# Kernel optimization log

Measured on AMD Instinct MI355X. Metric: run time of the kernel, lower is better.

The kernel has to match this reference:

```python
import jax, jax.numpy as jnp
import numpy as np

N, E, G = 5000, 10000, 200
EPS = 1e-5


def _nnconv(x, edge_attr, src, dst, w1, b1, w2, b2, root, bias, din, dout):
    # edge MLP -> per-edge weight matrix [E, din, dout]
    h = jax.nn.relu(edge_attr @ w1 + b1)
    We = (h @ w2 + b2).reshape(-1, din, dout)
    # gather source node feats, per-edge bmm, scatter-mean to targets
    msg = jnp.einsum('ei,eio->eo', x[src], We)  # [E, dout]
    s = jax.ops.segment_sum(msg, dst, num_segments=N)
    cnt = jax.ops.segment_sum(jnp.ones((msg.shape[0],), msg.dtype), dst, num_segments=N)
    agg = s / jnp.maximum(cnt, 1.0)[:, None]
    return agg + x @ root + bias


def _bn(x, g, b, m, v):
    return (x - m) * (g / jnp.sqrt(v + EPS)) + b


def setup_inputs() -> dict:
    key = jax.random.key(0)
    ks = iter(jax.random.split(key, 64))
    d = {}
    d['x'] = jax.random.normal(next(ks), (N, 15), jnp.float32)
    d['edge_attr'] = jax.random.normal(next(ks), (E, 3), jnp.float32)
    d['edge_index'] = jax.random.randint(next(ks), (2, E), 0, N, jnp.int32)
    d['batch'] = jnp.sort(jax.random.randint(next(ks), (N,), 0, G, jnp.int32))
    d['atom_num'] = jnp.zeros((G,), jnp.int32)
    dims = [(15, 64), (64, 128), (128, 256)]
    for l, (din, dout) in enumerate(dims, start=1):
        d[f'nn{l}_w1'] = jax.random.normal(next(ks), (3, 32), jnp.float32) * 0.1
        d[f'nn{l}_b1'] = jnp.zeros((32,), jnp.float32)
        d[f'nn{l}_w2'] = jax.random.normal(next(ks), (32, din * dout), jnp.float32) * 0.05
        d[f'nn{l}_b2'] = jnp.zeros((din * dout,), jnp.float32)
        d[f'root{l}'] = jax.random.normal(next(ks), (din, dout), jnp.float32) * 0.1
        d[f'bias{l}'] = jnp.zeros((dout,), jnp.float32)
        d[f'bn{l}_g'] = jnp.ones((dout,), jnp.float32)
        d[f'bn{l}_b'] = jnp.zeros((dout,), jnp.float32)
        d[f'bn{l}_m'] = jnp.zeros((dout,), jnp.float32)
        d[f'bn{l}_v'] = jnp.ones((dout,), jnp.float32)
    d['mlp_w'] = jax.random.normal(next(ks), (256, 200), jnp.float32) * 0.05
    d['mlp_b'] = jnp.zeros((200,), jnp.float32)
    return d


def reference(x, edge_attr, edge_index, batch, atom_num,
              nn1_w1, nn1_b1, nn1_w2, nn1_b2, root1, bias1, bn1_g, bn1_b, bn1_m, bn1_v,
              nn2_w1, nn2_b1, nn2_w2, nn2_b2, root2, bias2, bn2_g, bn2_b, bn2_m, bn2_v,
              nn3_w1, nn3_b1, nn3_w2, nn3_b2, root3, bias3, bn3_g, bn3_b, bn3_m, bn3_v,
              mlp_w, mlp_b):
    src, dst = edge_index[0], edge_index[1]
    h = _nnconv(x, edge_attr, src, dst, nn1_w1, nn1_b1, nn1_w2, nn1_b2, root1, bias1, 15, 64)
    h = jax.nn.relu(_bn(h, bn1_g, bn1_b, bn1_m, bn1_v))
    h = _nnconv(h, edge_attr, src, dst, nn2_w1, nn2_b1, nn2_w2, nn2_b2, root2, bias2, 64, 128)
    h = jax.nn.relu(_bn(h, bn2_g, bn2_b, bn2_m, bn2_v))
    h = _nnconv(h, edge_attr, src, dst, nn3_w1, nn3_b1, nn3_w2, nn3_b2, root3, bias3, 128, 256)
    h = jax.nn.relu(_bn(h, bn3_g, bn3_b, bn3_m, bn3_v))
    node_rep = h
    # per-graph node counts, exclusive cumulative offsets
    ones = jnp.ones((N,), h.dtype)
    counts = jax.ops.segment_sum(ones, batch, num_segments=G)  # [G]
    offsets = (jnp.cumsum(counts) - counts).astype(jnp.int32)
    idx = atom_num + offsets
    node_embedding = node_rep[idx]  # [G, 256]
    # global mean pool
    gsum = jax.ops.segment_sum(h, batch, num_segments=G)
    graph_embedding = gsum / jnp.maximum(counts, 1.0)[:, None]
    h_new = 0.5 * graph_embedding + node_embedding
    out = h_new @ mlp_w + mlp_b
    return out, node_embedding
```

## Files before the change

### kernel.cpp

```cpp
#include <hip/hip_runtime.h>
#include <stdint.h>

#define DEVINL __device__ __forceinline__

typedef __attribute__((ext_vector_type(8))) __bf16 bf16x8;
typedef __attribute__((ext_vector_type(8))) short s16x8;
typedef __attribute__((ext_vector_type(4))) float f32x4;

constexpr int NN = 5000;
constexpr int NE = 10000;
constexpr int NG = 200;
constexpr int BM = 64;
constexpr int MBLK = (NE + BM - 1) / BM;
constexpr int EROWS = MBLK * BM;
constexpr int NKP = 36;
constexpr int PHKT = 4;

DEVINL short f2bf(float f) {
  union { float f; unsigned u; } v; v.f = f;
  unsigned u = v.u + 0x7fffu + ((v.u >> 16) & 1u);
  return (short)(u >> 16);
}

DEVINL void gload16(const void* g, void* l) {
  __builtin_amdgcn_global_load_lds(
      (const __attribute__((address_space(1))) void*)g,
      (__attribute__((address_space(3))) void*)l, 16, 0, 0);
}


__global__ void prep(const int* dst, const int* batch, const float* x0,
                     float* cnt, float* gcnt, short* xbf0) {
  int idx = blockIdx.x * 256 + threadIdx.x;
  if (idx < NE) atomicAdd(&cnt[dst[idx]], 1.0f);
  if (idx < NN) atomicAdd(&gcnt[batch[idx]], 1.0f);
  if (idx < NN * 32) {
    int n = idx >> 5, i = idx & 31;
    xbf0[idx] = (i < 15) ? f2bf(x0[n * 15 + i]) : (short)0;
  }
}

__global__ void node_scan(const float* cnt, int* noff, int* fill) {
  __shared__ int s[1024];
  __shared__ int carry;
  int t = threadIdx.x;
  if (t == 0) carry = 0;
  __syncthreads();
  for (int c0 = 0; c0 < NN; c0 += 1024) {
    int i = c0 + t;
    int v = (i < NN) ? (int)cnt[i] : 0;
    s[t] = v;
    __syncthreads();
    for (int d = 1; d < 1024; d <<= 1) {
      int u = (t >= d) ? s[t - d] : 0;
      __syncthreads();
      s[t] += u;
      __syncthreads();
    }
    if (i < NN) { noff[i] = carry + s[t] - v; fill[i] = 0; }
    __syncthreads();
    if (t == 0) carry += s[1023];
    __syncthreads();
  }
}

__global__ void csr_fill(const int* dst, const int* noff, int* fill, int* elist) {
  int e = blockIdx.x * 256 + threadIdx.x;
  if (e < NE) {
    int n = dst[e];
    int p = noff[n] + atomicAdd(&fill[n], 1);
    elist[p] = e;
  }
}


__global__ void edge_mlp_all(const float* ea,
                             const float* w1a, const float* b1a,
                             const float* w1b, const float* b1b,
                             const float* w1c, const float* b1c,
                             short* hta, short* htb, short* htc) {
  int L = blockIdx.z;
  const float* w1 = (L == 0) ? w1a : (L == 1) ? w1b : w1c;
  const float* b1 = (L == 0) ? b1a : (L == 1) ? b1b : b1c;
  short* ht = (L == 0) ? hta : (L == 1) ? htb : htc;
  __shared__ float w1s[3];
  __shared__ float b1s;
  int t = threadIdx.x;
  int k = blockIdx.y;
  if (t < 3 && k < 32) w1s[t] = w1[t * 32 + k];
  if (t == 0 && k < 32) b1s = b1[k];
  __syncthreads();
  int e = blockIdx.x * 256 + t;
  if (e >= EROWS) return;
  float v = 0.f;
  if (e < NE) {
    if (k < 32) {
      float a = b1s + ea[e * 3] * w1s[0] + ea[e * 3 + 1] * w1s[1] +
                ea[e * 3 + 2] * w1s[2];
      v = a > 0.f ? a : 0.f;
    } else if (k == 32) {
      v = 1.0f;
    }
  }
  ht[(size_t)k * EROWS + e] = f2bf(v);
}


template <int DIN_DATA, int DIN_PAD, int DOUT>
DEVINL void buildB_one(int idx, const float* w2, const float* b2, short* Bp) {
  int cc = idx & 3;
  int n = (idx >> 2) % DOUT;
  int kt = (idx >> 2) / DOUT;
  int kap0 = kt * 32 + cc * 8;
  s16x8 v;
#pragma unroll
  for (int j = 0; j < 8; ++j) {
    int kap = kap0 + j;
    int k = kap / DIN_PAD, i = kap % DIN_PAD;
    float val = 0.f;
    if (i < DIN_DATA && k <= 32)
      val = (k < 32) ? w2[(size_t)(k * DIN_DATA + i) * DOUT + n]
                     : b2[(size_t)i * DOUT + n];
    v[j] = f2bf(val);
  }
  int swz = cc ^ ((n >> 1) & 3);
  *(s16x8*)((char*)Bp + (size_t)kt * DOUT * 64 + n * 64 + swz * 16) = v;
}

constexpr int BCH1 = (NKP * 32 / 8) * 64;
constexpr int BCH2 = (NKP * 64 / 8) * 128;
constexpr int BCH3 = (NKP * 128 / 8) * 256;

__global__ void build_B_all(const float* w2a, const float* b2a,
                            const float* w2b, const float* b2b,
                            const float* w2c, const float* b2c,
                            short* Bp1, short* Bp2, short* Bp3) {
  int idx = blockIdx.x * 256 + threadIdx.x;
  if (idx < BCH1) {
    buildB_one<15, 32, 64>(idx, w2a, b2a, Bp1);
  } else if (idx < BCH1 + BCH2) {
    buildB_one<64, 64, 128>(idx - BCH1, w2b, b2b, Bp2);
  } else if (idx < BCH1 + BCH2 + BCH3) {
    buildB_one<128, 128, 256>(idx - BCH1 - BCH2, w2c, b2c, Bp3);
  }
}


template <int DIN_PAD, int DOUT, int NSPLIT, int NKPE>
__launch_bounds__(512)
__global__ void fused_gemm(const short* xbf, const short* ht, const short* Bp,
                           const int* srcI, float* Pout) {
  constexpr int NI = DIN_PAD / 32;
  constexpr int ROWB = DIN_PAD * 2;
  constexpr int CHPR = ROWB / 16;
  constexpr int CHLOG = (CHPR == 4) ? 2 : (CHPR == 8) ? 3 : 4;
  constexpr int SWZM = (CHPR >= 8) ? 7 : 3;
  constexpr int DOUT_L = DOUT / NSPLIT;
  constexpr int MT = 2;
  constexpr int KT_TOTAL = NKPE * NI;
  constexpr int NPH = KT_TOTAL / PHKT;
  static_assert(KT_TOTAL % PHKT == 0, "phase align");
  static_assert(PHKT % NI == 0 || NI % PHKT == 0, "k align");
  constexpr int PHB = PHKT * DOUT_L * 64;
  constexpr int CPK = DOUT_L * 4;
  constexpr int CH = PHKT * CPK;
  constexpr int XGB = BM * ROWB;
  constexpr int SMB = (XGB > 2 * PHB) ? XGB : 2 * PHB;

  __shared__ __align__(16) char smem[SMB];
  __shared__ __align__(16) short hs[NKPE * BM];
  __shared__ int src_s[BM];

  const int t = threadIdx.x, lane = t & 63, w = t >> 6;
  const int wm = w >> 2, wn = w & 3;
  const int m0 = blockIdx.x * BM;
  const int bn0 = blockIdx.y * DOUT_L;
  if (t < BM) {
    int e = m0 + t;
    src_s[t] = (e < NE) ? srcI[e] : 0;
  }
  __syncthreads();

  constexpr int XCH = BM * CHPR;
#pragma unroll
  for (int rd = 0; rd < (XCH + 511) / 512; ++rd) {
    int L = rd * 512 + t;
    if (XCH % 512 == 0 || L < XCH) {
      int r = L >> CHLOG, pch = L & (CHPR - 1);
      int j = pch ^ (r & SWZM);
      gload16((const char*)xbf + (size_t)src_s[r] * ROWB + j * 16,
              (char*)smem + (size_t)L * 16);
    }
  }
  {
    int idx = t;
    if (idx < NKPE * (BM / 8)) {
      int kl = idx >> 3, c = idx & 7;
      gload16((const char*)ht + ((size_t)kl * EROWS + m0) * 2 + c * 16,
              (char*)hs + (size_t)idx * 16);
    }
  }
  __syncthreads();

  bf16x8 afr[NI][MT];
#pragma unroll
  for (int ii = 0; ii < NI; ++ii)
#pragma unroll
    for (int mt = 0; mt < MT; ++mt) {
      int r = wm * 32 + mt * 16 + (lane & 15);
      int c = ii * 4 + (lane >> 4);
      int pos = c ^ (r & SWZM);
      afr[ii][mt] = *(const bf16x8*)((const char*)smem + r * ROWB + pos * 16);
    }
  asm volatile("s_waitcnt lgkmcnt(0)" ::: "memory");
  __builtin_amdgcn_sched_barrier(0);
  __builtin_amdgcn_s_barrier();

  const char* Bg = (const char*)Bp + (size_t)bn0 * 64;
  auto stageB = [&](int ph, int buf) {
    char* dstB = (char*)smem + buf * PHB;
#pragma unroll
    for (int cc = 0; cc < CH / 512; ++cc) {
      int idx = cc * 512 + t;
      int ktl = idx / CPK;
      int win = idx % CPK;
      gload16(Bg + (size_t)(ph * PHKT + ktl) * (DOUT * 64) + (size_t)win * 16,
              dstB + (size_t)idx * 16);
    }
  };

  f32x4 msg[MT], part[MT];
#pragma unroll
  for (int mt = 0; mt < MT; ++mt)
#pragma unroll
    for (int i = 0; i < 4; ++i) { msg[mt][i] = 0.f; part[mt][i] = 0.f; }

  stageB(0, 0);
  int cur = 0;
  for (int ph = 0; ph < NPH; ++ph) {
    if (ph + 1 < NPH) {
      stageB(ph + 1, cur ^ 1);
      asm volatile("s_waitcnt vmcnt(2)" ::: "memory");
    } else {
      asm volatile("s_waitcnt vmcnt(0)" ::: "memory");
    }
    __builtin_amdgcn_s_barrier();
    __builtin_amdgcn_sched_barrier(0);
#pragma unroll
    for (int j = 0; j < PHKT; ++j) {
      const int kt = ph * PHKT + j;
      bf16x8 bfr;
      {
        int n = wn * 16 + (lane & 15);
        int cch = (lane >> 4) ^ ((n >> 1) & 3);
        bfr = *(const bf16x8*)((const char*)smem + cur * PHB +
                               j * (DOUT_L * 64) + n * 64 + cch * 16);
      }
#pragma unroll
      for (int mt = 0; mt < MT; ++mt)
        part[mt] = __builtin_amdgcn_mfma_f32_16x16x32_bf16(
            afr[j % NI][mt], bfr, part[mt], 0, 0, 0);
      if ((j % NI) == NI - 1) {
        int kl = kt / NI;
#pragma unroll
        for (int mt = 0; mt < MT; ++mt) {
          int rb = wm * 32 + mt * 16 + (lane >> 4) * 4;
          ushort4 hv = *(const ushort4*)((const char*)hs + (size_t)(kl * BM + rb) * 2);
          float h0, h1, h2, h3;
          { union { unsigned u; float f; } c;
            c.u = (unsigned)hv.x << 16; h0 = c.f;
            c.u = (unsigned)hv.y << 16; h1 = c.f;
            c.u = (unsigned)hv.z << 16; h2 = c.f;
            c.u = (unsigned)hv.w << 16; h3 = c.f; }
          msg[mt][0] += h0 * part[mt][0];
          msg[mt][1] += h1 * part[mt][1];
          msg[mt][2] += h2 * part[mt][2];
          msg[mt][3] += h3 * part[mt][3];
#pragma unroll
          for (int i = 0; i < 4; ++i) part[mt][i] = 0.f;
        }
      }
    }
    __builtin_amdgcn_sched_barrier(0);
    __builtin_amdgcn_s_barrier();
    cur ^= 1;
  }
  float* P = Pout + (size_t)m0 * DOUT + bn0;
#pragma unroll
  for (int mt = 0; mt < MT; ++mt) {
    int col = wn * 16 + (lane & 15);
#pragma unroll
    for (int reg = 0; reg < 4; ++reg) {
      int r = wm * 32 + mt * 16 + (lane >> 4) * 4 + reg;
      P[(size_t)r * DOUT + col] = msg[mt][reg];
    }
  }
}


template <int DIN, int DOUT>
__launch_bounds__(256)
__global__ void post_node(const float* P, const float* cnt, const int* noff,
                          const int* elist, const float* xin, const float* root,
                          const float* bias, const float* bg, const float* bb,
                          const float* bm, const float* bv, float* xout, short* xbf) {
  constexpr int NPB = 16;
  constexpr int OS = 256 / DOUT;
  constexpr int NPT = NPB / OS;
  __shared__ float xs[NPB * DIN];
  __shared__ int offs[NPB], cnts[NPB];
  int n0 = blockIdx.x * NPB;
  int t = threadIdx.x;
  int o = t % DOUT;
  int ng = t / DOUT;
  if (t < NPB) {
    int n = n0 + t;
    offs[t] = (n < NN) ? noff[n] : 0;
    cnts[t] = (n < NN) ? (int)cnt[n] : 0;
  }
  for (int idx = t; idx < NPB * DIN; idx += 256) {
    int n = n0 + idx / DIN;
    xs[idx] = (n < NN) ? xin[(size_t)n * DIN + idx % DIN] : 0.f;
  }
  __syncthreads();
  float acc[NPT];
#pragma unroll
  for (int q = 0; q < NPT; ++q) acc[q] = 0.f;
  for (int i = 0; i < DIN; ++i) {
    float rv = root[(size_t)i * DOUT + o];
#pragma unroll
    for (int q = 0; q < NPT; ++q) acc[q] += xs[(ng + q * OS) * DIN + i] * rv;
  }
  float bi = bias[o];
  float scale = bg[o] * rsqrtf(bv[o] + 1e-5f);
  float mo = bm[o], bo = bb[o];
#pragma unroll
  for (int q = 0; q < NPT; ++q) {
    int nn = ng + q * OS;
    int n = n0 + nn;
    if (n >= NN) continue;
    int off = offs[nn], c = cnts[nn];
    float s = 0.f;
    for (int j = 0; j < c; ++j) {
      int e = elist[off + j];
      s += P[(size_t)e * DOUT + o];
    }
    float accv = s / fmaxf((float)c, 1.f) + bi + acc[q];
    float v = (accv - mo) * scale + bo;
    v = v > 0.f ? v : 0.f;
    xout[(size_t)n * DOUT + o] = v;
    if (xbf) xbf[(size_t)n * DOUT + o] = f2bf(v);
  }
}


__global__ void finish(const float* gcnt, const int* atom, const float* x3,
                       const float* mw, const float* mb, float* out) {
  __shared__ float red[256];
  __shared__ float hnew[256];
  int g = blockIdx.x, t = threadIdx.x;
  red[t] = (t < NG && t < g) ? gcnt[t] : 0.f;
  __syncthreads();
#pragma unroll
  for (int d = 128; d > 0; d >>= 1) {
    if (t < d) red[t] += red[t + d];
    __syncthreads();
  }
  int st = (int)red[0];
  int cn = (int)gcnt[g];
  int id = st + atom[g];
  id = id < 0 ? 0 : (id > NN - 1 ? NN - 1 : id);
  float s = 0.f;
  for (int n = st; n < st + cn; ++n) s += x3[(size_t)n * 256 + t];
  float ge = s / fmaxf((float)cn, 1.f);
  float ne = x3[(size_t)id * 256 + t];
  out[40000 + g * 256 + t] = ne;
  hnew[t] = 0.5f * ge + ne;
  __syncthreads();
  if (t < 200) {
    float a = mb[t];
#pragma unroll 8
    for (int oo = 0; oo < 256; ++oo) a += hnew[oo] * mw[(size_t)oo * 200 + t];
    out[g * 200 + t] = a;
  }
}


template <int DIN_DATA, int DIN_PAD, int DOUT, int NSPLIT, int NKPE>
static void run_layer(void* const* d_in, int l, const int* srcI,
                      const short* xbf_in, const float* xin_f32, float* xout,
                      short* xbf_out, float* Pbuf, const float* cnt, const int* noff,
                      const int* elist, const short* ht, const short* Bp,
                      hipStream_t stream) {
  int base = 5 + (l - 1) * 10;
  const float* root = (const float*)d_in[base + 4];
  const float* bias = (const float*)d_in[base + 5];
  const float* bg = (const float*)d_in[base + 6];
  const float* bb = (const float*)d_in[base + 7];
  const float* bm = (const float*)d_in[base + 8];
  const float* bv = (const float*)d_in[base + 9];

  fused_gemm<DIN_PAD, DOUT, NSPLIT, NKPE>
      <<<dim3(MBLK, NSPLIT), 512, 0, stream>>>(xbf_in, ht, Bp, srcI, Pbuf);
  post_node<DIN_DATA, DOUT><<<(NN + 15) / 16, 256, 0, stream>>>(
      Pbuf, cnt, noff, elist, xin_f32, root, bias, bg, bb, bm, bv, xout, xbf_out);
}

extern "C" void kernel_launch(void* const* d_in, const int* in_sizes, int n_in,
                              void* d_out, int out_size, void* d_ws, size_t ws_size,
                              hipStream_t stream) {
  (void)in_sizes; (void)n_in; (void)out_size; (void)ws_size;
  const float* x0 = (const float*)d_in[0];
  const float* ea = (const float*)d_in[1];
  const int* eidx = (const int*)d_in[2];
  const int* batch = (const int*)d_in[3];
  const int* atom = (const int*)d_in[4];
  const float* mw = (const float*)d_in[35];
  const float* mb = (const float*)d_in[36];
  const int* srcI = eidx;
  const int* dstI = eidx + NE;
  float* out = (float*)d_out;

  char* p = (char*)d_ws;
  auto alloc = [&](size_t bytes) {
    char* r = p;
    p += (bytes + 255) & ~size_t(255);
    return r;
  };
  float* xA = (float*)alloc((size_t)NN * 256 * 4);
  float* xB = (float*)alloc((size_t)NN * 256 * 4);
  float* Pbuf = (float*)alloc((size_t)EROWS * 256 * 4);
  float* cnt = (float*)alloc(NN * 4);
  int* noff = (int*)alloc(NN * 4);
  int* fill = (int*)alloc(NN * 4);
  int* elist = (int*)alloc(NE * 4);
  float* gcnt = (float*)alloc(NG * 4);
  short* ht1 = (short*)alloc((size_t)NKP * EROWS * 2);
  short* ht2 = (short*)alloc((size_t)NKP * EROWS * 2);
  short* ht3 = (short*)alloc((size_t)NKP * EROWS * 2);
  short* Bp1 = (short*)alloc((size_t)NKP * 32 * 64 * 2);
  short* Bp2 = (short*)alloc((size_t)NKP * 64 * 128 * 2);
  short* Bp3 = (short*)alloc((size_t)NKP * 128 * 256 * 2);
  short* xbf0 = (short*)alloc((size_t)NN * 32 * 2);
  short* xbfA = (short*)alloc((size_t)NN * 64 * 2);
  short* xbfB = (short*)alloc((size_t)NN * 128 * 2);

  hipMemsetAsync(cnt, 0, NN * 4, stream);
  hipMemsetAsync(gcnt, 0, NG * 4, stream);
  prep<<<(NN * 32 + 255) / 256, 256, 0, stream>>>(dstI, batch, x0, cnt, gcnt, xbf0);
  node_scan<<<1, 1024, 0, stream>>>(cnt, noff, fill);
  csr_fill<<<(NE + 255) / 256, 256, 0, stream>>>(dstI, noff, fill, elist);
  edge_mlp_all<<<dim3((EROWS + 255) / 256, NKP, 3), 256, 0, stream>>>(
      ea, (const float*)d_in[5], (const float*)d_in[6],
      (const float*)d_in[15], (const float*)d_in[16],
      (const float*)d_in[25], (const float*)d_in[26], ht1, ht2, ht3);
  build_B_all<<<(BCH1 + BCH2 + BCH3 + 255) / 256, 256, 0, stream>>>(
      (const float*)d_in[7], (const float*)d_in[8],
      (const float*)d_in[17], (const float*)d_in[18],
      (const float*)d_in[27], (const float*)d_in[28], Bp1, Bp2, Bp3);

  run_layer<15, 32, 64, 1, 36>(d_in, 1, srcI, xbf0, x0, xA, xbfA, Pbuf, cnt,
                               noff, elist, ht1, Bp1, stream);
  run_layer<64, 64, 128, 2, 34>(d_in, 2, srcI, xbfA, xA, xB, xbfB, Pbuf, cnt,
                                noff, elist, ht2, Bp2, stream);
  run_layer<128, 128, 256, 4, 33>(d_in, 3, srcI, xbfB, xB, xA, (short*)nullptr,
                                  Pbuf, cnt, noff, elist, ht3, Bp3, stream);

  finish<<<NG, 256, 0, stream>>>(gcnt, atom, xA, mw, mb, out);
}
```

Measured before the change: 303.4 us.

## Fold root linear term into fused GEMM as extra self-row blocks

The node root projection x @ root moves out of the scalar post_node loop into the MFMA GEMM. Root weights are packed as an extra K slice (k==33) of the B operand, and extra self blocks compute x·root per node into an extended P buffer. post_node now just reads the self row and drops its shared-memory x staging, uses 8 nodes per block, and skips the fp32 output for intermediate layers. The root multiply now runs in bf16 rather than fp32, which may lose some precision, and more GEMM blocks are launched.

After: 271.5 us. 10.5% less time.

```diff
diff --git a/kernel.cpp b/kernel.cpp
--- a/kernel.cpp
+++ b/kernel.cpp
@@ -13,6 +13,8 @@
 constexpr int BM = 64;
 constexpr int MBLK = (NE + BM - 1) / BM;
 constexpr int EROWS = MBLK * BM;
+constexpr int SBLK = (NN + BM - 1) / BM;
+constexpr int SROWS = SBLK * BM;
 constexpr int NKP = 36;
 constexpr int PHKT = 4;
 
@@ -107,7 +109,8 @@
 
 
 template <int DIN_DATA, int DIN_PAD, int DOUT>
-DEVINL void buildB_one(int idx, const float* w2, const float* b2, short* Bp) {
+DEVINL void buildB_one(int idx, const float* w2, const float* b2,
+                       const float* root, short* Bp) {
   int cc = idx & 3;
   int n = (idx >> 2) % DOUT;
   int kt = (idx >> 2) / DOUT;
@@ -118,9 +121,10 @@
     int kap = kap0 + j;
     int k = kap / DIN_PAD, i = kap % DIN_PAD;
     float val = 0.f;
-    if (i < DIN_DATA && k <= 32)
+    if (i < DIN_DATA && k <= 33)
       val = (k < 32) ? w2[(size_t)(k * DIN_DATA + i) * DOUT + n]
-                     : b2[(size_t)i * DOUT + n];
+                     : (k == 32) ? b2[(size_t)i * DOUT + n]
+                                 : root[(size_t)i * DOUT + n];
     v[j] = f2bf(val);
   }
   int swz = cc ^ ((n >> 1) & 3);
@@ -131,17 +135,17 @@
 constexpr int BCH2 = (NKP * 64 / 8) * 128;
 constexpr int BCH3 = (NKP * 128 / 8) * 256;
 
-__global__ void build_B_all(const float* w2a, const float* b2a,
-                            const float* w2b, const float* b2b,
-                            const float* w2c, const float* b2c,
+__global__ void build_B_all(const float* w2a, const float* b2a, const float* ra,
+                            const float* w2b, const float* b2b, const float* rb,
+                            const float* w2c, const float* b2c, const float* rc,
                             short* Bp1, short* Bp2, short* Bp3) {
   int idx = blockIdx.x * 256 + threadIdx.x;
   if (idx < BCH1) {
-    buildB_one<15, 32, 64>(idx, w2a, b2a, Bp1);
+    buildB_one<15, 32, 64>(idx, w2a, b2a, ra, Bp1);
   } else if (idx < BCH1 + BCH2) {
-    buildB_one<64, 64, 128>(idx - BCH1, w2b, b2b, Bp2);
+    buildB_one<64, 64, 128>(idx - BCH1, w2b, b2b, rb, Bp2);
   } else if (idx < BCH1 + BCH2 + BCH3) {
-    buildB_one<128, 128, 256>(idx - BCH1 - BCH2, w2c, b2c, Bp3);
+    buildB_one<128, 128, 256>(idx - BCH1 - BCH2, w2c, b2c, rc, Bp3);
   }
 }
 
@@ -173,11 +177,12 @@
 
   const int t = threadIdx.x, lane = t & 63, w = t >> 6;
   const int wm = w >> 2, wn = w & 3;
-  const int m0 = blockIdx.x * BM;
+  const bool isSelf = (blockIdx.x >= MBLK);
+  const int m0 = (isSelf ? (blockIdx.x - MBLK) : blockIdx.x) * BM;
   const int bn0 = blockIdx.y * DOUT_L;
   if (t < BM) {
-    int e = m0 + t;
-    src_s[t] = (e < NE) ? srcI[e] : 0;
+    int r = m0 + t;
+    src_s[t] = isSelf ? ((r < NN) ? r : 0) : ((r < NE) ? srcI[r] : 0);
   }
   __syncthreads();
 
@@ -192,13 +197,10 @@
               (char*)smem + (size_t)L * 16);
     }
   }
-  {
-    int idx = t;
-    if (idx < NKPE * (BM / 8)) {
-      int kl = idx >> 3, c = idx & 7;
-      gload16((const char*)ht + ((size_t)kl * EROWS + m0) * 2 + c * 16,
-              (char*)hs + (size_t)idx * 16);
-    }
+  if (!isSelf && t < NKPE * (BM / 8)) {
+    int kl = t >> 3, c = t & 7;
+    gload16((const char*)ht + ((size_t)kl * EROWS + m0) * 2 + c * 16,
+            (char*)hs + (size_t)t * 16);
   }
   __syncthreads();
 
@@ -217,6 +219,55 @@
   __builtin_amdgcn_s_barrier();
 
   const char* Bg = (const char*)Bp + (size_t)bn0 * 64;
+
+  f32x4 msg[MT], part[MT];
+#pragma unroll
+  for (int mt = 0; mt < MT; ++mt)
+#pragma unroll
+    for (int i = 0; i < 4; ++i) { msg[mt][i] = 0.f; part[mt][i] = 0.f; }
+
+  if (isSelf) {
+    constexpr int KT0 = 33 * NI;
+    constexpr int CHS = NI * CPK;
+#pragma unroll
+    for (int cc = 0; cc < (CHS + 511) / 512; ++cc) {
+      int idx = cc * 512 + t;
+      if (CHS % 512 == 0 || idx < CHS) {
+        int ktl = idx / CPK, win = idx % CPK;
+        gload16(Bg + (size_t)(KT0 + ktl) * (DOUT * 64) + (size_t)win * 16,
+                (char*)smem + (size_t)idx * 16);
+      }
+    }
+    asm volatile("s_waitcnt vmcnt(0)" ::: "memory");
+    __builtin_amdgcn_s_barrier();
+    __builtin_amdgcn_sched_barrier(0);
+#pragma unroll
+    for (int j = 0; j < NI; ++j) {
+      bf16x8 bfr;
+      {
+        int n = wn * 16 + (lane & 15);
+        int cch = (lane >> 4) ^ ((n >> 1) & 3);
+        bfr = *(const bf16x8*)((const char*)smem + j * (DOUT_L * 64) + n * 64 +
+                               cch * 16);
+      }
+#pragma unroll
+      for (int mt = 0; mt < MT; ++mt)
+        msg[mt] = __builtin_amdgcn_mfma_f32_16x16x32_bf16(afr[j][mt], bfr,
+                                                          msg[mt], 0, 0, 0);
+    }
+    float* P = Pout + (size_t)(EROWS + m0) * DOUT + bn0;
+#pragma unroll
+    for (int mt = 0; mt < MT; ++mt) {
+      int col = wn * 16 + (lane & 15);
+#pragma unroll
+      for (int reg = 0; reg < 4; ++reg) {
+        int r = wm * 32 + mt * 16 + (lane >> 4) * 4 + reg;
+        P[(size_t)r * DOUT + col] = msg[mt][reg];
+      }
+    }
+    return;
+  }
+
   auto stageB = [&](int ph, int buf) {
     char* dstB = (char*)smem + buf * PHB;
 #pragma unroll
@@ -228,12 +279,6 @@
               dstB + (size_t)idx * 16);
     }
   };
-
-  f32x4 msg[MT], part[MT];
-#pragma unroll
-  for (int mt = 0; mt < MT; ++mt)
-#pragma unroll
-    for (int i = 0; i < 4; ++i) { msg[mt][i] = 0.f; part[mt][i] = 0.f; }
 
   stageB(0, 0);
   int cur = 0;
@@ -298,16 +343,15 @@
 }
 
 
-template <int DIN, int DOUT>
+template <int DOUT>
 __launch_bounds__(256)
 __global__ void post_node(const float* P, const float* cnt, const int* noff,
-                          const int* elist, const float* xin, const float* root,
-                          const float* bias, const float* bg, const float* bb,
-                          const float* bm, const float* bv, float* xout, short* xbf) {
-  constexpr int NPB = 16;
+                          const int* elist, const float* bias, const float* bg,
+                          const float* bb, const float* bm, const float* bv,
+                          float* xout, short* xbf) {
+  constexpr int NPB = 8;
   constexpr int OS = 256 / DOUT;
   constexpr int NPT = NPB / OS;
-  __shared__ float xs[NPB * DIN];
   __shared__ int offs[NPB], cnts[NPB];
   int n0 = blockIdx.x * NPB;
   int t = threadIdx.x;
@@ -318,19 +362,7 @@
     offs[t] = (n < NN) ? noff[n] : 0;
     cnts[t] = (n < NN) ? (int)cnt[n] : 0;
   }
-  for (int idx = t; idx < NPB * DIN; idx += 256) {
-    int n = n0 + idx / DIN;
-    xs[idx] = (n < NN) ? xin[(size_t)n * DIN + idx % DIN] : 0.f;
-  }
-  __syncthreads();
-  float acc[NPT];
-#pragma unroll
-  for (int q = 0; q < NPT; ++q) acc[q] = 0.f;
-  for (int i = 0; i < DIN; ++i) {
-    float rv = root[(size_t)i * DOUT + o];
-#pragma unroll
-    for (int q = 0; q < NPT; ++q) acc[q] += xs[(ng + q * OS) * DIN + i] * rv;
-  }
+  __syncthreads();
   float bi = bias[o];
   float scale = bg[o] * rsqrtf(bv[o] + 1e-5f);
   float mo = bm[o], bo = bb[o];
@@ -345,10 +377,11 @@
       int e = elist[off + j];
       s += P[(size_t)e * DOUT + o];
     }
-    float accv = s / fmaxf((float)c, 1.f) + bi + acc[q];
+    float selfv = P[(size_t)(EROWS + n) * DOUT + o];
+    float accv = s / fmaxf((float)c, 1.f) + selfv + bi;
     float v = (accv - mo) * scale + bo;
     v = v > 0.f ? v : 0.f;
-    xout[(size_t)n * DOUT + o] = v;
+    if (xout) xout[(size_t)n * DOUT + o] = v;
     if (xbf) xbf[(size_t)n * DOUT + o] = f2bf(v);
   }
 }
@@ -386,14 +419,13 @@
 }
 
 
-template <int DIN_DATA, int DIN_PAD, int DOUT, int NSPLIT, int NKPE>
+template <int DIN_PAD, int DOUT, int NSPLIT, int NKPE>
 static void run_layer(void* const* d_in, int l, const int* srcI,
-                      const short* xbf_in, const float* xin_f32, float* xout,
-                      short* xbf_out, float* Pbuf, const float* cnt, const int* noff,
+                      const short* xbf_in, float* xout_f32, short* xbf_out,
+                      float* Pbuf, const float* cnt, const int* noff,
                       const int* elist, const short* ht, const short* Bp,
                       hipStream_t stream) {
   int base = 5 + (l - 1) * 10;
-  const float* root = (const float*)d_in[base + 4];
   const float* bias = (const float*)d_in[base + 5];
   const float* bg = (const float*)d_in[base + 6];
   const float* bb = (const float*)d_in[base + 7];
@@ -401,9 +433,9 @@
   const float* bv = (const float*)d_in[base + 9];
 
   fused_gemm<DIN_PAD, DOUT, NSPLIT, NKPE>
-      <<<dim3(MBLK, NSPLIT), 512, 0, stream>>>(xbf_in, ht, Bp, srcI, Pbuf);
-  post_node<DIN_DATA, DOUT><<<(NN + 15) / 16, 256, 0, stream>>>(
-      Pbuf, cnt, noff, elist, xin_f32, root, bias, bg, bb, bm, bv, xout, xbf_out);
+      <<<dim3(MBLK + SBLK, NSPLIT), 512, 0, stream>>>(xbf_in, ht, Bp, srcI, Pbuf);
+  post_node<DOUT><<<(NN + 7) / 8, 256, 0, stream>>>(
+      Pbuf, cnt, noff, elist, bias, bg, bb, bm, bv, xout_f32, xbf_out);
 }
 
 extern "C" void kernel_launch(void* const* d_in, const int* in_sizes, int n_in,
@@ -428,8 +460,7 @@
     return r;
   };
   float* xA = (float*)alloc((size_t)NN * 256 * 4);
-  float* xB = (float*)alloc((size_t)NN * 256 * 4);
-  float* Pbuf = (float*)alloc((size_t)EROWS * 256 * 4);
+  float* Pbuf = (float*)alloc((size_t)(EROWS + SROWS) * 256 * 4);
   float* cnt = (float*)alloc(NN * 4);
   int* noff = (int*)alloc(NN * 4);
   int* fill = (int*)alloc(NN * 4);
@@ -455,16 +486,17 @@
       (const float*)d_in[15], (const float*)d_in[16],
       (const float*)d_in[25], (const float*)d_in[26], ht1, ht2, ht3);
   build_B_all<<<(BCH1 + BCH2 + BCH3 + 255) / 256, 256, 0, stream>>>(
-      (const float*)d_in[7], (const float*)d_in[8],
-      (const float*)d_in[17], (const float*)d_in[18],
-      (const float*)d_in[27], (const float*)d_in[28], Bp1, Bp2, Bp3);
-
-  run_layer<15, 32, 64, 1, 36>(d_in, 1, srcI, xbf0, x0, xA, xbfA, Pbuf, cnt,
-                               noff, elist, ht1, Bp1, stream);
-  run_layer<64, 64, 128, 2, 34>(d_in, 2, srcI, xbfA, xA, xB, xbfB, Pbuf, cnt,
-                                noff, elist, ht2, Bp2, stream);
-  run_layer<128, 128, 256, 4, 33>(d_in, 3, srcI, xbfB, xB, xA, (short*)nullptr,
-                                  Pbuf, cnt, noff, elist, ht3, Bp3, stream);
+      (const float*)d_in[7], (const float*)d_in[8], (const float*)d_in[9],
+      (const float*)d_in[17], (const float*)d_in[18], (const float*)d_in[19],
+      (const float*)d_in[27], (const float*)d_in[28], (const float*)d_in[29],
+      Bp1, Bp2, Bp3);
+
+  run_layer<32, 64, 1, 36>(d_in, 1, srcI, xbf0, (float*)nullptr, xbfA, Pbuf,
+                           cnt, noff, elist, ht1, Bp1, stream);
+  run_layer<64, 128, 2, 34>(d_in, 2, srcI, xbfA, (float*)nullptr, xbfB, Pbuf,
+                            cnt, noff, elist, ht2, Bp2, stream);
+  run_layer<128, 256, 4, 33>(d_in, 3, srcI, xbfB, xA, (short*)nullptr, Pbuf,
+                             cnt, noff, elist, ht3, Bp3, stream);
 
   finish<<<NG, 256, 0, stream>>>(gcnt, atom, xA, mw, mb, out);
 }
```
